# Kernel optimization log

Hardware: AMD Instinct MI355X
Metric: run time of the kernel (lower is better)

The kernel has to match this reference:

```python
import jax, jax.numpy as jnp
import numpy as np

N = 1048576  # number of frequency sampling points
K = 64       # number of cascaded SVF sections


def setup_inputs() -> dict:
    key = jax.random.key(0)
    ks = jax.random.split(key, 7)
    return {
        "x_real": jax.random.normal(ks[0], (N,), dtype=jnp.float32),
        "x_imag": jax.random.normal(ks[1], (N,), dtype=jnp.float32),
        "f":   jax.random.normal(ks[2], (1, K), dtype=jnp.float32),
        "R":   jax.random.normal(ks[3], (1, K), dtype=jnp.float32),
        "mLP": jax.random.normal(ks[4], (1, K), dtype=jnp.float32),
        "mBP": jax.random.normal(ks[5], (1, K), dtype=jnp.float32),
        "mHP": jax.random.normal(ks[6], (1, K), dtype=jnp.float32),
    }


def reference(x_real, x_imag, f, R, mLP, mBP, mHP):
    # x: complex sampling points (z on / near the unit circle)
    x = jax.lax.complex(x_real, x_imag)  # [N] complex64
    f, R, mLP, mBP, mHP = f[0], R[0], mLP[0], mBP[0], mHP[0]  # [K]
    f2 = f * f
    # biquad coefficients, [3, K]
    beta = jnp.stack([
        f2 * mLP + f * mBP + mHP,
        2.0 * f2 * mLP - 2.0 * mHP,
        f2 * mLP - f * mBP + mHP,
    ])
    alpha = jnp.stack([
        f2 + 2.0 * R * f + 1.0,
        2.0 * f2 - 2.0,
        f2 - 2.0 * R * f + 1.0,
    ])
    # X = [x^0, x^-1, x^-2], [N, 3] complex
    xinv = 1.0 / x
    X = jnp.stack([jnp.ones_like(x), xinv, xinv * xinv], axis=1)
    num = X @ beta.astype(X.dtype)    # [N, K]
    den = X @ alpha.astype(X.dtype)   # [N, K]
    # original initializes H = 1 + 1j then multiplies all K sections
    H = (1.0 + 1.0j) * jnp.prod(num / den, axis=1)  # [N]
    return H
```

## Files before the change

### kernel.cpp

```cpp
#include <hip/hip_runtime.h>


#define NSEC  64
#define NOCT  16
#define BLOCK 256
#define MPT   2

__global__ __launch_bounds__(64) void svf_coef_v11(
    const float* __restrict__ f_g,  const float* __restrict__ R_g,
    const float* __restrict__ lp_g, const float* __restrict__ bp_g,
    const float* __restrict__ hp_g,
    float* __restrict__ coef)
{
    const int t = threadIdx.x;
    if (t >= NOCT) return;

    double qn[2][5], qd[2][5];
    for (int s = 0; s < 2; ++s) {
        const int k0 = 4 * t + 2 * s, k1 = k0 + 1;
        double fk = (double)f_g[k0],  Rk = (double)R_g[k0];
        double lp = (double)lp_g[k0], bp = (double)bp_g[k0], hp = (double)hp_g[k0];
        double f2 = fk * fk, fbp = fk * bp, flp = f2 * lp, rf2 = 2.0 * Rk * fk;
        const double b0 = flp + fbp + hp, b1 = 2.0 * flp - 2.0 * hp, b2 = flp - fbp + hp;
        const double a0 = f2 + rf2 + 1.0, a1 = 2.0 * f2 - 2.0,       a2 = f2 - rf2 + 1.0;
        fk = (double)f_g[k1];  Rk = (double)R_g[k1];
        lp = (double)lp_g[k1]; bp = (double)bp_g[k1]; hp = (double)hp_g[k1];
        f2 = fk * fk; fbp = fk * bp; flp = f2 * lp; rf2 = 2.0 * Rk * fk;
        const double B0 = flp + fbp + hp, B1 = 2.0 * flp - 2.0 * hp, B2 = flp - fbp + hp;
        const double A0 = f2 + rf2 + 1.0, A1 = 2.0 * f2 - 2.0,       A2 = f2 - rf2 + 1.0;
        qn[s][0] = b0 * B0;
        qn[s][1] = b0 * B1 + b1 * B0;
        qn[s][2] = b0 * B2 + b1 * B1 + b2 * B0;
        qn[s][3] = b1 * B2 + b2 * B1;
        qn[s][4] = b2 * B2;
        qd[s][0] = a0 * A0;
        qd[s][1] = a0 * A1 + a1 * A0;
        qd[s][2] = a0 * A2 + a1 * A1 + a2 * A0;
        qd[s][3] = a1 * A2 + a2 * A1;
        qd[s][4] = a2 * A2;
    }
    double en[9], ed[9];
    for (int j = 0; j < 9; ++j) { en[j] = 0.0; ed[j] = 0.0; }
    for (int i = 0; i < 5; ++i)
        for (int j = 0; j < 5; ++j) {
            en[i + j] += qn[0][i] * qn[1][j];
            ed[i + j] += qd[0][i] * qd[1][j];
        }
    float* cp = coef + t * 18;
    for (int j = 0; j < 9; ++j) {
        cp[j]     = (float)en[j];
        cp[9 + j] = (float)ed[j];
    }
}

__global__ __launch_bounds__(BLOCK) void svf_f32_v11(
    const float* __restrict__ xr_g, const float* __restrict__ xi_g,
    const float* __restrict__ coef,
    float* __restrict__ out, int n, long long cap_floats)
{
    const int t = threadIdx.x;
    const long long base = (long long)(blockIdx.x * BLOCK + t) * MPT;

    float X1r[MPT], X1i[MPT], X2r[MPT], X2i[MPT], X3r[MPT], X3i[MPT];
    float X4r[MPT], X4i[MPT], X5r[MPT], X5i[MPT], X6r[MPT], X6i[MPT];
    float X7r[MPT], X7i[MPT], X8r[MPT], X8i[MPT];
    float Hr[MPT], Hi[MPT];

    if (base + MPT <= (long long)n) {
        const float2 a = *reinterpret_cast<const float2*>(xr_g + base);
        const float2 b = *reinterpret_cast<const float2*>(xi_g + base);
        X1r[0] = a.x; X1r[1] = a.y;
        X1i[0] = b.x; X1i[1] = b.y;
    } else {
        for (int m = 0; m < MPT; ++m) {
            const long long idx = base + m;
            const bool ok = idx < (long long)n;
            X1r[m] = ok ? xr_g[idx] : 1.0f;
            X1i[m] = ok ? xi_g[idx] : 0.0f;
        }
    }

    #pragma unroll
    for (int m = 0; m < MPT; ++m) {
        X2r[m] = fmaf(X1r[m], X1r[m], -(X1i[m] * X1i[m]));
        X2i[m] = 2.0f * X1r[m] * X1i[m];
        X3r[m] = fmaf(X2r[m], X1r[m], -(X2i[m] * X1i[m]));
        X3i[m] = fmaf(X2r[m], X1i[m],   X2i[m] * X1r[m]);
        X4r[m] = fmaf(X2r[m], X2r[m], -(X2i[m] * X2i[m]));
        X4i[m] = 2.0f * X2r[m] * X2i[m];
        X5r[m] = fmaf(X4r[m], X1r[m], -(X4i[m] * X1i[m]));
        X5i[m] = fmaf(X4r[m], X1i[m],   X4i[m] * X1r[m]);
        X6r[m] = fmaf(X3r[m], X3r[m], -(X3i[m] * X3i[m]));
        X6i[m] = 2.0f * X3r[m] * X3i[m];
        X7r[m] = fmaf(X4r[m], X3r[m], -(X4i[m] * X3i[m]));
        X7i[m] = fmaf(X4r[m], X3i[m],   X4i[m] * X3r[m]);
        X8r[m] = fmaf(X4r[m], X4r[m], -(X4i[m] * X4i[m]));
        X8i[m] = 2.0f * X4r[m] * X4i[m];
        Hr[m] = 1.0f;
        Hi[m] = 1.0f;
    }

    #pragma unroll
    for (int p = 0; p < NOCT; ++p) {
        const float* cp = coef + p * 18;
        const float e0 = cp[0], e1 = cp[1], e2 = cp[2], e3 = cp[3], e4 = cp[4];
        const float e5 = cp[5], e6 = cp[6], e7 = cp[7], e8 = cp[8];
        const float g0 = cp[9], g1 = cp[10], g2 = cp[11], g3 = cp[12], g4 = cp[13];
        const float g5 = cp[14], g6 = cp[15], g7 = cp[16], g8 = cp[17];
        #pragma unroll
        for (int m = 0; m < MPT; ++m) {
            const float nr = fmaf(e0, X8r[m], fmaf(e1, X7r[m], fmaf(e2, X6r[m],
                             fmaf(e3, X5r[m], fmaf(e4, X4r[m], fmaf(e5, X3r[m],
                             fmaf(e6, X2r[m], fmaf(e7, X1r[m], e8))))))));
            const float ni = fmaf(e0, X8i[m], fmaf(e1, X7i[m], fmaf(e2, X6i[m],
                             fmaf(e3, X5i[m], fmaf(e4, X4i[m], fmaf(e5, X3i[m],
                             fmaf(e6, X2i[m], e7 * X1i[m])))))));
            const float dr = fmaf(g0, X8r[m], fmaf(g1, X7r[m], fmaf(g2, X6r[m],
                             fmaf(g3, X5r[m], fmaf(g4, X4r[m], fmaf(g5, X3r[m],
                             fmaf(g6, X2r[m], fmaf(g7, X1r[m], g8))))))));
            const float di = fmaf(g0, X8i[m], fmaf(g1, X7i[m], fmaf(g2, X6i[m],
                             fmaf(g3, X5i[m], fmaf(g4, X4i[m], fmaf(g5, X3i[m],
                             fmaf(g6, X2i[m], g7 * X1i[m])))))));
            const float dd  = fmaf(dr, dr, di * di);
            const float inv = __builtin_amdgcn_rcpf(dd);
            const float tr  = fmaf(nr, dr,   ni * di);
            const float ti  = fmaf(ni, dr, -(nr * di));
            const float rr  = tr * inv;
            const float ri  = ti * inv;
            const float hr = fmaf(Hr[m], rr, -(Hi[m] * ri));
            const float hi = fmaf(Hr[m], ri,   Hi[m] * rr);
            Hr[m] = hr; Hi[m] = hi;
        }
    }

    const long long imag_off = (long long)n;
    if (base + MPT <= (long long)n && 2LL * (long long)n <= cap_floats) {
        float2 vr, vi;
        vr.x = Hr[0]; vr.y = Hr[1];
        vi.x = Hi[0]; vi.y = Hi[1];
        *reinterpret_cast<float2*>(out + base)            = vr;
        *reinterpret_cast<float2*>(out + imag_off + base) = vi;
    } else {
        for (int m = 0; m < MPT; ++m) {
            const long long idx = base + m;
            if (idx < (long long)n) {
                if (idx + 1 <= cap_floats) out[idx] = Hr[m];
                const long long oi = imag_off + idx;
                if (oi + 1 <= cap_floats) out[oi] = Hi[m];
            }
        }
    }
}

extern "C" void kernel_launch(void* const* d_in, const int* in_sizes, int n_in,
                              void* d_out, int out_size, void* d_ws, size_t ws_size,
                              hipStream_t stream) {
    const float* xr = (const float*)d_in[0];
    const float* xi = (const float*)d_in[1];
    const float* f  = (const float*)d_in[2];
    const float* R  = (const float*)d_in[3];
    const float* lp = (const float*)d_in[4];
    const float* bp = (const float*)d_in[5];
    const float* hp = (const float*)d_in[6];
    float* out = (float*)d_out;
    float* coef = (float*)d_ws;

    const int n = in_sizes[0];
    long long cap = (long long)out_size;
    if (cap > 2LL * (long long)n) cap = 2LL * (long long)n;

    svf_coef_v11<<<1, 64, 0, stream>>>(f, R, lp, bp, hp, coef);
    const int grid = (n + BLOCK * MPT - 1) / (BLOCK * MPT);
    svf_f32_v11<<<grid, BLOCK, 0, stream>>>(xr, xi, coef, out, n, cap);
}
```

Baseline: 82.89 us.

## Merge sections into degree-16 polynomials to halve complex divisions

The coefficient kernel now multiplies eight biquad sections per thread into degree-16 numerator and denominator polynomials in double precision. It rescales each pair by a power of two taken from the denominator's largest coefficient before writing float coefficients. The main kernel computes powers x^1..x^16 and evaluates 8 rational factors instead of 16, cutting the reciprocals and complex multiplies per point. This raises register pressure (launch bounds request 4 blocks) and risks float precision loss when evaluating high-degree polynomials, especially for |x| far from 1.

```diff
diff --git a/kernel.cpp b/kernel.cpp
--- a/kernel.cpp
+++ b/kernel.cpp
@@ -2,58 +2,76 @@
 
 
 #define NSEC  64
-#define NOCT  16
+#define NHEX  8
+#define DEG   16
+#define NCF   34
 #define BLOCK 256
 #define MPT   2
 
-__global__ __launch_bounds__(64) void svf_coef_v11(
+__global__ __launch_bounds__(64) void svf_coef_v13(
     const float* __restrict__ f_g,  const float* __restrict__ R_g,
     const float* __restrict__ lp_g, const float* __restrict__ bp_g,
     const float* __restrict__ hp_g,
     float* __restrict__ coef)
 {
     const int t = threadIdx.x;
-    if (t >= NOCT) return;
+    if (t >= NHEX) return;
 
-    double qn[2][5], qd[2][5];
-    for (int s = 0; s < 2; ++s) {
-        const int k0 = 4 * t + 2 * s, k1 = k0 + 1;
-        double fk = (double)f_g[k0],  Rk = (double)R_g[k0];
-        double lp = (double)lp_g[k0], bp = (double)bp_g[k0], hp = (double)hp_g[k0];
-        double f2 = fk * fk, fbp = fk * bp, flp = f2 * lp, rf2 = 2.0 * Rk * fk;
-        const double b0 = flp + fbp + hp, b1 = 2.0 * flp - 2.0 * hp, b2 = flp - fbp + hp;
-        const double a0 = f2 + rf2 + 1.0, a1 = 2.0 * f2 - 2.0,       a2 = f2 - rf2 + 1.0;
-        fk = (double)f_g[k1];  Rk = (double)R_g[k1];
-        lp = (double)lp_g[k1]; bp = (double)bp_g[k1]; hp = (double)hp_g[k1];
-        f2 = fk * fk; fbp = fk * bp; flp = f2 * lp; rf2 = 2.0 * Rk * fk;
-        const double B0 = flp + fbp + hp, B1 = 2.0 * flp - 2.0 * hp, B2 = flp - fbp + hp;
-        const double A0 = f2 + rf2 + 1.0, A1 = 2.0 * f2 - 2.0,       A2 = f2 - rf2 + 1.0;
-        qn[s][0] = b0 * B0;
-        qn[s][1] = b0 * B1 + b1 * B0;
-        qn[s][2] = b0 * B2 + b1 * B1 + b2 * B0;
-        qn[s][3] = b1 * B2 + b2 * B1;
-        qn[s][4] = b2 * B2;
-        qd[s][0] = a0 * A0;
-        qd[s][1] = a0 * A1 + a1 * A0;
-        qd[s][2] = a0 * A2 + a1 * A1 + a2 * A0;
-        qd[s][3] = a1 * A2 + a2 * A1;
-        qd[s][4] = a2 * A2;
+    double pn[DEG + 1], pd[DEG + 1];
+    #pragma unroll
+    for (int j = 0; j <= DEG; ++j) { pn[j] = 0.0; pd[j] = 0.0; }
+    pn[0] = 1.0; pd[0] = 1.0;
+
+    #pragma unroll
+    for (int s = 0; s < 8; ++s) {
+        const int k = 8 * t + s;
+        const double fk = (double)f_g[k],  Rk = (double)R_g[k];
+        const double lp = (double)lp_g[k], bp = (double)bp_g[k], hp = (double)hp_g[k];
+        const double f2 = fk * fk, fbp = fk * bp, flp = f2 * lp, rf2 = 2.0 * Rk * fk;
+        const double bb0 = flp - fbp + hp;
+        const double bb1 = 2.0 * flp - 2.0 * hp;
+        const double bb2 = flp + fbp + hp;
+        const double aa0 = f2 - rf2 + 1.0;
+        const double aa1 = 2.0 * f2 - 2.0;
+        const double aa2 = f2 + rf2 + 1.0;
+
+        double nn[DEG + 1], nd[DEG + 1];
+        #pragma unroll
+        for (int j = 0; j <= DEG; ++j) { nn[j] = 0.0; nd[j] = 0.0; }
+        #pragma unroll
+        for (int i = 0; i <= DEG - 2; ++i) {
+            nn[i]     += pn[i] * bb0;
+            nn[i + 1] += pn[i] * bb1;
+            nn[i + 2] += pn[i] * bb2;
+            nd[i]     += pd[i] * aa0;
+            nd[i + 1] += pd[i] * aa1;
+            nd[i + 2] += pd[i] * aa2;
+        }
+        #pragma unroll
+        for (int j = 0; j <= DEG; ++j) { pn[j] = nn[j]; pd[j] = nd[j]; }
     }
-    double en[9], ed[9];
-    for (int j = 0; j < 9; ++j) { en[j] = 0.0; ed[j] = 0.0; }
-    for (int i = 0; i < 5; ++i)
-        for (int j = 0; j < 5; ++j) {
-            en[i + j] += qn[0][i] * qn[1][j];
-            ed[i + j] += qd[0][i] * qd[1][j];
-        }
-    float* cp = coef + t * 18;
-    for (int j = 0; j < 9; ++j) {
-        cp[j]     = (float)en[j];
-        cp[9 + j] = (float)ed[j];
+
+    double mx = 0.0;
+    #pragma unroll
+    for (int j = 0; j <= DEG; ++j) mx = fmax(mx, fabs(pd[j]));
+    const double sc = (mx > 0.0) ? ldexp(1.0, -ilogb(mx)) : 1.0;
+
+    float* cp = coef + t * NCF;
+    #pragma unroll
+    for (int j = 0; j <= DEG; ++j) {
+        cp[j]          = (float)(pn[j] * sc);
+        cp[17 + j]     = (float)(pd[j] * sc);
     }
 }
 
-__global__ __launch_bounds__(BLOCK) void svf_f32_v11(
+#define CSQ(dr_, di_, ar_, ai_)                                   \
+    dr_ = fmaf((ar_), (ar_), -((ai_) * (ai_)));                   \
+    di_ = 2.0f * ((ar_) * (ai_));
+#define CMUL(dr_, di_, ar_, ai_, br_, bi_)                        \
+    dr_ = fmaf((ar_), (br_), -((ai_) * (bi_)));                   \
+    di_ = fmaf((ar_), (bi_),  ((ai_) * (br_)));
+
+__global__ __launch_bounds__(BLOCK, 4) void svf_f32_v13(
     const float* __restrict__ xr_g, const float* __restrict__ xi_g,
     const float* __restrict__ coef,
     float* __restrict__ out, int n, long long cap_floats)
@@ -61,66 +79,61 @@
     const int t = threadIdx.x;
     const long long base = (long long)(blockIdx.x * BLOCK + t) * MPT;
 
-    float X1r[MPT], X1i[MPT], X2r[MPT], X2i[MPT], X3r[MPT], X3i[MPT];
-    float X4r[MPT], X4i[MPT], X5r[MPT], X5i[MPT], X6r[MPT], X6i[MPT];
-    float X7r[MPT], X7i[MPT], X8r[MPT], X8i[MPT];
+    float Xr[16][MPT], Xi[16][MPT];
     float Hr[MPT], Hi[MPT];
 
     if (base + MPT <= (long long)n) {
         const float2 a = *reinterpret_cast<const float2*>(xr_g + base);
         const float2 b = *reinterpret_cast<const float2*>(xi_g + base);
-        X1r[0] = a.x; X1r[1] = a.y;
-        X1i[0] = b.x; X1i[1] = b.y;
+        Xr[0][0] = a.x; Xr[0][1] = a.y;
+        Xi[0][0] = b.x; Xi[0][1] = b.y;
     } else {
         for (int m = 0; m < MPT; ++m) {
             const long long idx = base + m;
             const bool ok = idx < (long long)n;
-            X1r[m] = ok ? xr_g[idx] : 1.0f;
-            X1i[m] = ok ? xi_g[idx] : 0.0f;
+            Xr[0][m] = ok ? xr_g[idx] : 1.0f;
+            Xi[0][m] = ok ? xi_g[idx] : 0.0f;
         }
     }
 
     #pragma unroll
     for (int m = 0; m < MPT; ++m) {
-        X2r[m] = fmaf(X1r[m], X1r[m], -(X1i[m] * X1i[m]));
-        X2i[m] = 2.0f * X1r[m] * X1i[m];
-        X3r[m] = fmaf(X2r[m], X1r[m], -(X2i[m] * X1i[m]));
-        X3i[m] = fmaf(X2r[m], X1i[m],   X2i[m] * X1r[m]);
-        X4r[m] = fmaf(X2r[m], X2r[m], -(X2i[m] * X2i[m]));
-        X4i[m] = 2.0f * X2r[m] * X2i[m];
-        X5r[m] = fmaf(X4r[m], X1r[m], -(X4i[m] * X1i[m]));
-        X5i[m] = fmaf(X4r[m], X1i[m],   X4i[m] * X1r[m]);
-        X6r[m] = fmaf(X3r[m], X3r[m], -(X3i[m] * X3i[m]));
-        X6i[m] = 2.0f * X3r[m] * X3i[m];
-        X7r[m] = fmaf(X4r[m], X3r[m], -(X4i[m] * X3i[m]));
-        X7i[m] = fmaf(X4r[m], X3i[m],   X4i[m] * X3r[m]);
-        X8r[m] = fmaf(X4r[m], X4r[m], -(X4i[m] * X4i[m]));
-        X8i[m] = 2.0f * X4r[m] * X4i[m];
+        CSQ (Xr[1][m],  Xi[1][m],  Xr[0][m], Xi[0][m]);
+        CMUL(Xr[2][m],  Xi[2][m],  Xr[1][m], Xi[1][m], Xr[0][m], Xi[0][m]);
+        CSQ (Xr[3][m],  Xi[3][m],  Xr[1][m], Xi[1][m]);
+        CMUL(Xr[4][m],  Xi[4][m],  Xr[3][m], Xi[3][m], Xr[0][m], Xi[0][m]);
+        CSQ (Xr[5][m],  Xi[5][m],  Xr[2][m], Xi[2][m]);
+        CMUL(Xr[6][m],  Xi[6][m],  Xr[3][m], Xi[3][m], Xr[2][m], Xi[2][m]);
+        CSQ (Xr[7][m],  Xi[7][m],  Xr[3][m], Xi[3][m]);
+        CMUL(Xr[8][m],  Xi[8][m],  Xr[7][m], Xi[7][m], Xr[0][m], Xi[0][m]);
+        CSQ (Xr[9][m],  Xi[9][m],  Xr[4][m], Xi[4][m]);
+        CMUL(Xr[10][m], Xi[10][m], Xr[7][m], Xi[7][m], Xr[2][m], Xi[2][m]);
+        CSQ (Xr[11][m], Xi[11][m], Xr[5][m], Xi[5][m]);
+        CMUL(Xr[12][m], Xi[12][m], Xr[7][m], Xi[7][m], Xr[4][m], Xi[4][m]);
+        CSQ (Xr[13][m], Xi[13][m], Xr[6][m], Xi[6][m]);
+        CMUL(Xr[14][m], Xi[14][m], Xr[7][m], Xi[7][m], Xr[6][m], Xi[6][m]);
+        CSQ (Xr[15][m], Xi[15][m], Xr[7][m], Xi[7][m]);
         Hr[m] = 1.0f;
         Hi[m] = 1.0f;
     }
 
     #pragma unroll
-    for (int p = 0; p < NOCT; ++p) {
-        const float* cp = coef + p * 18;
-        const float e0 = cp[0], e1 = cp[1], e2 = cp[2], e3 = cp[3], e4 = cp[4];
-        const float e5 = cp[5], e6 = cp[6], e7 = cp[7], e8 = cp[8];
-        const float g0 = cp[9], g1 = cp[10], g2 = cp[11], g3 = cp[12], g4 = cp[13];
-        const float g5 = cp[14], g6 = cp[15], g7 = cp[16], g8 = cp[17];
+    for (int p = 0; p < NHEX; ++p) {
+        const float* cp = coef + p * NCF;
+        float cn[17], cd[17];
+        #pragma unroll
+        for (int j = 0; j < 17; ++j) { cn[j] = cp[j]; cd[j] = cp[17 + j]; }
+
         #pragma unroll
         for (int m = 0; m < MPT; ++m) {
-            const float nr = fmaf(e0, X8r[m], fmaf(e1, X7r[m], fmaf(e2, X6r[m],
-                             fmaf(e3, X5r[m], fmaf(e4, X4r[m], fmaf(e5, X3r[m],
-                             fmaf(e6, X2r[m], fmaf(e7, X1r[m], e8))))))));
-            const float ni = fmaf(e0, X8i[m], fmaf(e1, X7i[m], fmaf(e2, X6i[m],
-                             fmaf(e3, X5i[m], fmaf(e4, X4i[m], fmaf(e5, X3i[m],
-                             fmaf(e6, X2i[m], e7 * X1i[m])))))));
-            const float dr = fmaf(g0, X8r[m], fmaf(g1, X7r[m], fmaf(g2, X6r[m],
-                             fmaf(g3, X5r[m], fmaf(g4, X4r[m], fmaf(g5, X3r[m],
-                             fmaf(g6, X2r[m], fmaf(g7, X1r[m], g8))))))));
-            const float di = fmaf(g0, X8i[m], fmaf(g1, X7i[m], fmaf(g2, X6i[m],
-                             fmaf(g3, X5i[m], fmaf(g4, X4i[m], fmaf(g5, X3i[m],
-                             fmaf(g6, X2i[m], g7 * X1i[m])))))));
+            float nr = cn[0], ni = 0.0f, dr = cd[0], di = 0.0f;
+            #pragma unroll
+            for (int q = 1; q <= 16; ++q) {
+                nr = fmaf(cn[q], Xr[q - 1][m], nr);
+                ni = fmaf(cn[q], Xi[q - 1][m], ni);
+                dr = fmaf(cd[q], Xr[q - 1][m], dr);
+                di = fmaf(cd[q], Xi[q - 1][m], di);
+            }
             const float dd  = fmaf(dr, dr, di * di);
             const float inv = __builtin_amdgcn_rcpf(dd);
             const float tr  = fmaf(nr, dr,   ni * di);
@@ -169,7 +182,7 @@
     long long cap = (long long)out_size;
     if (cap > 2LL * (long long)n) cap = 2LL * (long long)n;
 
-    svf_coef_v11<<<1, 64, 0, stream>>>(f, R, lp, bp, hp, coef);
+    svf_coef_v13<<<1, 64, 0, stream>>>(f, R, lp, bp, hp, coef);
     const int grid = (n + BLOCK * MPT - 1) / (BLOCK * MPT);
-    svf_f32_v11<<<grid, BLOCK, 0, stream>>>(xr, xi, coef, out, n, cap);
+    svf_f32_v13<<<grid, BLOCK, 0, stream>>>(xr, xi, coef, out, n, cap);
 }
```

After: 83.69 us. Within noise of the previous version (+1.0%).
